# Kernel tuning notes

Hardware: AMD Instinct MI355X
Metric: run time of the kernel (lower is better)

## Reference

```python
import jax, jax.numpy as jnp
import numpy as np

B, L, INPUT_DIM = 2, 2048, 512
D_MODEL, N_HEAD, MLP_HIDDEN = 1024, 16, 4096
CONTEXT_LENGTH = 2048
EPS = 1e-5


def _layer_norm(x, w, b):
    mu = jnp.mean(x, axis=-1, keepdims=True)
    var = jnp.mean(jnp.square(x - mu), axis=-1, keepdims=True)
    return (x - mu) * jax.lax.rsqrt(var + EPS) * w + b


def setup_inputs() -> dict:
    key = jax.random.key(0)
    ks = jax.random.split(key, 12)
    s = 0.02
    return {
        "x": jax.random.normal(ks[0], (B, L, INPUT_DIM), dtype=jnp.float32),
        "wte_w": jax.random.normal(ks[1], (INPUT_DIM, D_MODEL), dtype=jnp.float32) * s,
        "wte_b": jnp.zeros((D_MODEL,), dtype=jnp.float32),
        "wpe": jax.random.normal(ks[2], (CONTEXT_LENGTH, D_MODEL), dtype=jnp.float32) * s,
        "ln1_w": jnp.ones((D_MODEL,), dtype=jnp.float32),
        "ln1_b": jnp.zeros((D_MODEL,), dtype=jnp.float32),
        "kq_w": jax.random.normal(ks[3], (D_MODEL, 2 * D_MODEL), dtype=jnp.float32) * s,
        "kq_b": jnp.zeros((2 * D_MODEL,), dtype=jnp.float32),
        "v_w": jax.random.normal(ks[4], (D_MODEL, D_MODEL), dtype=jnp.float32) * s,
        "v_b": jnp.zeros((D_MODEL,), dtype=jnp.float32),
        "ao_w": jax.random.normal(ks[5], (D_MODEL, D_MODEL), dtype=jnp.float32) * s,
        "ao_b": jnp.zeros((D_MODEL,), dtype=jnp.float32),
        "ln2_w": jnp.ones((D_MODEL,), dtype=jnp.float32),
        "ln2_b": jnp.zeros((D_MODEL,), dtype=jnp.float32),
        "fc_w": jax.random.normal(ks[6], (D_MODEL, MLP_HIDDEN), dtype=jnp.float32) * s,
        "fc_b": jnp.zeros((MLP_HIDDEN,), dtype=jnp.float32),
        "proj_w": jax.random.normal(ks[7], (MLP_HIDDEN, INPUT_DIM), dtype=jnp.float32) * s,
        "proj_b": jnp.zeros((INPUT_DIM,), dtype=jnp.float32),
    }


def reference(x, wte_w, wte_b, wpe, ln1_w, ln1_b, kq_w, kq_b, v_w, v_b,
              ao_w, ao_b, ln2_w, ln2_b, fc_w, fc_b, proj_w, proj_b):
    b, l, _ = x.shape
    hd = D_MODEL // N_HEAD
    # token "embedding" (linear) + learnable positional embedding
    h = x @ wte_w + wte_b + wpe[:l]                      # [B, L, D]
    hn = _layer_norm(h, ln1_w, ln1_b)                    # ln_1
    # attention (kq fused linear -> split gives k first, then q)
    kq = hn @ kq_w + kq_b                                # [B, L, 2D]
    k, q = kq[..., :D_MODEL], kq[..., D_MODEL:]
    v = hn @ v_w + v_b
    q = q.reshape(b, l, N_HEAD, hd).transpose(0, 2, 1, 3)  # [B, H, L, hd]
    k = k.reshape(b, l, N_HEAD, hd).transpose(0, 2, 1, 3)
    v = v.reshape(b, l, N_HEAD, hd).transpose(0, 2, 1, 3)
    scale = 1.0 / jnp.sqrt(jnp.asarray(hd, dtype=q.dtype))
    scores = jnp.einsum('bhqd,bhkd->bhqk', q, k) * scale  # [B, H, L, L]
    causal = jnp.tril(jnp.ones((l, l), dtype=bool))
    scores = jnp.where(causal, scores, jnp.asarray(-jnp.inf, dtype=scores.dtype))
    attn = jax.nn.softmax(scores, axis=-1)
    o = jnp.einsum('bhqk,bhkd->bhqd', attn, v)            # [B, H, L, hd]
    o = o.transpose(0, 2, 1, 3).reshape(b, l, D_MODEL)
    o = o @ ao_w + ao_b
    attn_out = hn + o                                     # residual recorded by Block
    xo = _layer_norm(attn_out, ln2_w, ln2_b)              # ln_2
    # MLP head to input_dim (exact GELU, matching torch nn.GELU default)
    out = jax.nn.gelu(xo @ fc_w + fc_b, approximate=False) @ proj_w + proj_b
    return (out, attn_out)
```

## Files before the change

### kernel.cpp

```cpp
#include <hip/hip_runtime.h>
#include <hip/hip_bf16.h>
#include <cmath>

#define D_MODEL   1024
#define N_HEAD    16
#define HEAD_DIM  64
#define SEQ_LEN   2048
#define NBATCH    2
#define M_TOTAL   (NBATCH * SEQ_LEN)
#define IN_DIM    512
#define MLP_HID   4096

typedef __attribute__((ext_vector_type(8))) short short8;
typedef __attribute__((ext_vector_type(4))) short short4v;
typedef __attribute__((ext_vector_type(4))) float floatx4;

typedef const __attribute__((address_space(1))) void* gas_ptr;
typedef __attribute__((address_space(3))) void* las_ptr;

__device__ __forceinline__ void async_copy16(const void* g, void* l) {
  __builtin_amdgcn_global_load_lds((gas_ptr)g, (las_ptr)l, 16, 0, 0);
}


__global__ __launch_bounds__(256) void k_convert_bf16(const float* __restrict__ in,
                                                      __hip_bfloat16* __restrict__ out,
                                                      int n4) {
  int i = blockIdx.x * 256 + threadIdx.x;
  if (i >= n4) return;
  float4 v = ((const float4*)in)[i];
  int base = i * 4;
  out[base + 0] = __float2bfloat16(v.x);
  out[base + 1] = __float2bfloat16(v.y);
  out[base + 2] = __float2bfloat16(v.z);
  out[base + 3] = __float2bfloat16(v.w);
}

__global__ __launch_bounds__(256) void k_reduce_proj(const __hip_bfloat16* __restrict__ part,
                                                     const float* __restrict__ bias,
                                                     float* __restrict__ out) {
  int i = blockIdx.x * 256 + threadIdx.x;
  const size_t SP = (size_t)M_TOTAL * IN_DIM / 4;
  float4 s = ((const float4*)bias)[i & (IN_DIM / 4 - 1)];
#pragma unroll
  for (int j = 0; j < 8; j++) {
    short4v v = ((const short4v*)part)[i + j * SP];
    s.x += __bfloat162float(((const __hip_bfloat16*)&v)[0]);
    s.y += __bfloat162float(((const __hip_bfloat16*)&v)[1]);
    s.z += __bfloat162float(((const __hip_bfloat16*)&v)[2]);
    s.w += __bfloat162float(((const __hip_bfloat16*)&v)[3]);
  }
  ((float4*)out)[i] = s;
}

__global__ __launch_bounds__(256) void k_transpose_bf16(const float* __restrict__ in,
                                                        __hip_bfloat16* __restrict__ out,
                                                        int K, int N) {
  __shared__ float tile[32][33];
  int n0 = blockIdx.x * 32, k0 = blockIdx.y * 32;
  int tx = threadIdx.x & 31, ty = threadIdx.x >> 5;
#pragma unroll
  for (int i = 0; i < 32; i += 8)
    tile[ty + i][tx] = in[(size_t)(k0 + ty + i) * N + n0 + tx];
  __syncthreads();
#pragma unroll
  for (int i = 0; i < 32; i += 8)
    out[(size_t)(n0 + ty + i) * K + k0 + tx] = __float2bfloat16(tile[tx][ty + i]);
}

__global__ __launch_bounds__(256) void k_transpose_v(const __hip_bfloat16* __restrict__ in,
                                                     __hip_bfloat16* __restrict__ out) {
  __shared__ __hip_bfloat16 t[64][72];
  int bh = blockIdx.y;
  int l0 = blockIdx.x * 64;
  in  += (size_t)bh * SEQ_LEN * HEAD_DIM;
  out += (size_t)bh * HEAD_DIM * SEQ_LEN;
  int tx = threadIdx.x & 7, ty = threadIdx.x >> 3;
#pragma unroll
  for (int i = 0; i < 64; i += 32) {
    short8 v = *(const short8*)(in + (size_t)(l0 + ty + i) * HEAD_DIM + tx * 8);
#pragma unroll
    for (int j = 0; j < 8; j++) t[ty + i][tx * 8 + j] = ((__hip_bfloat16*)&v)[j];
  }
  __syncthreads();
#pragma unroll
  for (int i = 0; i < 64; i += 32) {
    int d = ty + i;
    short8 o;
#pragma unroll
    for (int j = 0; j < 8; j++) ((__hip_bfloat16*)&o)[j] = t[tx * 8 + j][d];
    *(short8*)(out + (size_t)d * SEQ_LEN + l0 + tx * 8) = o;
  }
}


__global__ __launch_bounds__(256) void k_ln1_combine(const float* __restrict__ part,
                                                     const float* __restrict__ wb,
                                                     const float* __restrict__ wpe,
                                                     const float* __restrict__ lw,
                                                     const float* __restrict__ lb,
                                                     __hip_bfloat16* __restrict__ out_bf) {
  int row = blockIdx.x;
  int l = row & (SEQ_LEN - 1);
  float4 a = ((const float4*)(part + (size_t)row * D_MODEL))[threadIdx.x];
  float4 c = ((const float4*)(part + (size_t)(M_TOTAL + row) * D_MODEL))[threadIdx.x];
  float4 wb4 = ((const float4*)wb)[threadIdx.x];
  float4 pe4 = ((const float4*)(wpe + (size_t)l * D_MODEL))[threadIdx.x];
  float4 v;
  v.x = a.x + c.x + wb4.x + pe4.x;
  v.y = a.y + c.y + wb4.y + pe4.y;
  v.z = a.z + c.z + wb4.z + pe4.z;
  v.w = a.w + c.w + wb4.w + pe4.w;
  float s  = v.x + v.y + v.z + v.w;
  float sq = v.x * v.x + v.y * v.y + v.z * v.z + v.w * v.w;
#pragma unroll
  for (int o = 1; o < 64; o <<= 1) { s += __shfl_xor(s, o); sq += __shfl_xor(sq, o); }
  __shared__ float ss[4], ssq[4];
  int lane = threadIdx.x & 63, wv = threadIdx.x >> 6;
  if (lane == 0) { ss[wv] = s; ssq[wv] = sq; }
  __syncthreads();
  s  = ss[0] + ss[1] + ss[2] + ss[3];
  sq = ssq[0] + ssq[1] + ssq[2] + ssq[3];
  float mu  = s * (1.f / D_MODEL);
  float var = sq * (1.f / D_MODEL) - mu * mu;
  float rs  = rsqrtf(var + 1e-5f);
  float4 lw4 = ((const float4*)lw)[threadIdx.x];
  float4 lb4 = ((const float4*)lb)[threadIdx.x];
  size_t base = (size_t)row * D_MODEL + threadIdx.x * 4;
  out_bf[base + 0] = __float2bfloat16((v.x - mu) * rs * lw4.x + lb4.x);
  out_bf[base + 1] = __float2bfloat16((v.y - mu) * rs * lw4.y + lb4.y);
  out_bf[base + 2] = __float2bfloat16((v.z - mu) * rs * lw4.z + lb4.z);
  out_bf[base + 3] = __float2bfloat16((v.w - mu) * rs * lw4.w + lb4.w);
}

__global__ __launch_bounds__(256) void k_ln2_combine(const float* __restrict__ part,
                                                     const float* __restrict__ bias,
                                                     const __hip_bfloat16* __restrict__ hn,
                                                     const float* __restrict__ lw,
                                                     const float* __restrict__ lb,
                                                     float* __restrict__ attn_out,
                                                     __hip_bfloat16* __restrict__ out_bf) {
  int row = blockIdx.x;
  float4 a = ((const float4*)(part + (size_t)row * D_MODEL))[threadIdx.x];
  float4 c = ((const float4*)(part + (size_t)(M_TOTAL + row) * D_MODEL))[threadIdx.x];
  float4 b4 = ((const float4*)bias)[threadIdx.x];
  short4v h4 = ((const short4v*)(hn + (size_t)row * D_MODEL))[threadIdx.x];
  float4 v;
  v.x = a.x + c.x + b4.x + __bfloat162float(((const __hip_bfloat16*)&h4)[0]);
  v.y = a.y + c.y + b4.y + __bfloat162float(((const __hip_bfloat16*)&h4)[1]);
  v.z = a.z + c.z + b4.z + __bfloat162float(((const __hip_bfloat16*)&h4)[2]);
  v.w = a.w + c.w + b4.w + __bfloat162float(((const __hip_bfloat16*)&h4)[3]);
  ((float4*)(attn_out + (size_t)row * D_MODEL))[threadIdx.x] = v;
  float s  = v.x + v.y + v.z + v.w;
  float sq = v.x * v.x + v.y * v.y + v.z * v.z + v.w * v.w;
#pragma unroll
  for (int o = 1; o < 64; o <<= 1) { s += __shfl_xor(s, o); sq += __shfl_xor(sq, o); }
  __shared__ float ss[4], ssq[4];
  int lane = threadIdx.x & 63, wv = threadIdx.x >> 6;
  if (lane == 0) { ss[wv] = s; ssq[wv] = sq; }
  __syncthreads();
  s  = ss[0] + ss[1] + ss[2] + ss[3];
  sq = ssq[0] + ssq[1] + ssq[2] + ssq[3];
  float mu  = s * (1.f / D_MODEL);
  float var = sq * (1.f / D_MODEL) - mu * mu;
  float rs  = rsqrtf(var + 1e-5f);
  float4 lw4 = ((const float4*)lw)[threadIdx.x];
  float4 lb4 = ((const float4*)lb)[threadIdx.x];
  size_t base = (size_t)row * D_MODEL + threadIdx.x * 4;
  out_bf[base + 0] = __float2bfloat16((v.x - mu) * rs * lw4.x + lb4.x);
  out_bf[base + 1] = __float2bfloat16((v.y - mu) * rs * lw4.y + lb4.y);
  out_bf[base + 2] = __float2bfloat16((v.z - mu) * rs * lw4.z + lb4.z);
  out_bf[base + 3] = __float2bfloat16((v.w - mu) * rs * lw4.w + lb4.w);
}


struct KQVEpi {
  const float* kq_b; const float* v_b;
  __hip_bfloat16* kb; __hip_bfloat16* qb; __hip_bfloat16* vb;
  __device__ void operator()(int row, int col, float v) const {
    int b = row >> 11, l = row & (SEQ_LEN - 1);
    int which = col >> 10, c = col & (D_MODEL - 1);
    float t = v + ((which == 2) ? v_b[c] : kq_b[col]);
    if (which == 1) t *= 0.125f;
    int head = c >> 6, d = c & 63;
    __hip_bfloat16* dst = (which == 0) ? kb : (which == 1) ? qb : vb;
    dst[(((size_t)(b * N_HEAD + head) * SEQ_LEN) + l) * HEAD_DIM + d] = __float2bfloat16(t);
  }
};

struct FCEpi {
  const float* bias; __hip_bfloat16* act;
  __device__ void operator()(int row, int col, float v) const {
    float t = v + bias[col];
    float g = 0.5f * t * (1.f + erff(t * 0.70710678118654752f));
    act[(size_t)row * MLP_HID + col] = __float2bfloat16(g);
  }
};

struct PartEpi {
  float* part;
  __device__ void operator()(int row, int col, float v) const {
    part[(size_t)blockIdx.z * ((size_t)M_TOTAL * D_MODEL) + (size_t)row * D_MODEL + col] = v;
  }
};

struct PartBf16Epi {
  __hip_bfloat16* part;
  __device__ void operator()(int row, int col, float v) const {
    part[(size_t)blockIdx.z * ((size_t)M_TOTAL * IN_DIM) + (size_t)row * IN_DIM + col] =
        __float2bfloat16(v);
  }
};


template <class Epi>
__global__ __launch_bounds__(256) void k_gemm(const __hip_bfloat16* __restrict__ A,
                                              const __hip_bfloat16* __restrict__ Bt,
                                              int M, int N, int K, int Kchunk, Epi epi) {
  __shared__ __align__(16) short As[128 * 64];
  __shared__ __align__(16) short Bs[128 * 64];
  const int tid  = threadIdx.x;
  const int lane = tid & 63;
  const int w    = tid >> 6;
  const int wm   = (w >> 1) << 6;
  const int wn   = (w & 1) << 6;
  const int r    = lane & 15;
  const int quad = lane >> 4;
  const int m0 = blockIdx.y << 7;
  const int n0 = blockIdx.x << 7;
  const int koff = blockIdx.z * Kchunk;

  const __hip_bfloat16* pa[4];
  const __hip_bfloat16* pb[4];
#pragma unroll
  for (int j = 0; j < 4; j++) {
    int s = tid + j * 256;
    int row = s >> 3;
    int c = (s & 7) ^ (row & 7);
    pa[j] = A  + (size_t)(m0 + row) * K + (c << 3) + koff;
    pb[j] = Bt + (size_t)(n0 + row) * K + (c << 3) + koff;
  }

  floatx4 acc[4][4];
#pragma unroll
  for (int i = 0; i < 4; i++)
#pragma unroll
    for (int j = 0; j < 4; j++) acc[i][j] = (floatx4){0.f, 0.f, 0.f, 0.f};

  int aoff[2][4], boff[2][4];
#pragma unroll
  for (int kk = 0; kk < 2; kk++)
#pragma unroll
    for (int i = 0; i < 4; i++) {
      int pc = ((quad + (kk << 2)) ^ (r & 7)) << 3;
      aoff[kk][i] = (wm + i * 16 + r) * 64 + pc;
      boff[kk][i] = (wn + i * 16 + r) * 64 + pc;
    }

  for (int k0 = 0; k0 < Kchunk; k0 += 64) {
    __syncthreads();
#pragma unroll
    for (int j = 0; j < 4; j++) {
      async_copy16(pa[j] + k0, &As[(tid + j * 256) * 8]);
      async_copy16(pb[j] + k0, &Bs[(tid + j * 256) * 8]);
    }
    __syncthreads();
#pragma unroll
    for (int kk = 0; kk < 2; kk++) {
      short8 fa[4], fb[4];
#pragma unroll
      for (int i = 0; i < 4; i++) {
        fa[i] = *(const short8*)&As[aoff[kk][i]];
        fb[i] = *(const short8*)&Bs[boff[kk][i]];
      }
#pragma unroll
      for (int i = 0; i < 4; i++)
#pragma unroll
        for (int j = 0; j < 4; j++)
          acc[i][j] = __builtin_amdgcn_mfma_f32_16x16x32_bf16(fa[i], fb[j], acc[i][j], 0, 0, 0);
    }
  }

#pragma unroll
  for (int i = 0; i < 4; i++)
#pragma unroll
    for (int j = 0; j < 4; j++) {
      int row = m0 + wm + i * 16 + quad * 4;
      int col = n0 + wn + j * 16 + r;
#pragma unroll
      for (int t = 0; t < 4; t++) epi(row + t, col, acc[i][j][t]);
    }
}

template <class Epi>
static void launch_gemm(const __hip_bfloat16* A, const __hip_bfloat16* Bt,
                        int M, int N, int K, Epi epi, hipStream_t s) {
  dim3 grid(N / 128, M / 128, 1);
  k_gemm<Epi><<<grid, 256, 0, s>>>(A, Bt, M, N, K, K, epi);
}


#define PSTR 68

__global__ __launch_bounds__(256) void k_flash_attn(const __hip_bfloat16* __restrict__ kb,
                                                    const __hip_bfloat16* __restrict__ qb,
                                                    const __hip_bfloat16* __restrict__ vtb,
                                                    __hip_bfloat16* __restrict__ ob) {
  __shared__ __align__(16) short Ks[64 * 64];
  __shared__ __align__(16) short Vs[64 * 64];
  __shared__ __align__(16) __hip_bfloat16 Pb[4][2][16 * PSTR];
  const int tid  = threadIdx.x;
  const int lane = tid & 63;
  const int w    = tid >> 6;
  const int r    = lane & 15;
  const int quad = lane >> 4;
  const int bh    = blockIdx.x & 31;
  const int strip = (SEQ_LEN / 128 - 1) - (blockIdx.x >> 5);
  const int qb0   = strip << 7;
  const int qbw   = qb0 + (w << 5);
  const int qend  = qbw + 32;
  const int b = bh >> 4, h = bh & (N_HEAD - 1);

  const __hip_bfloat16* qp = qb  + ((size_t)bh * SEQ_LEN + qbw) * HEAD_DIM;
  const __hip_bfloat16* kp = kb  + (size_t)bh * SEQ_LEN * HEAD_DIM;
  const __hip_bfloat16* vp = vtb + (size_t)bh * HEAD_DIM * SEQ_LEN;
  __hip_bfloat16* pw0 = &Pb[w][0][0];
  __hip_bfloat16* pw1 = &Pb[w][1][0];

  short8 qf[2][2];
  qf[0][0] = *(const short8*)(qp + r * HEAD_DIM + quad * 8);
  qf[0][1] = *(const short8*)(qp + r * HEAD_DIM + quad * 8 + 32);
  qf[1][0] = *(const short8*)(qp + (16 + r) * HEAD_DIM + quad * 8);
  qf[1][1] = *(const short8*)(qp + (16 + r) * HEAD_DIM + quad * 8 + 32);

  floatx4 of[2][4];
#pragma unroll
  for (int f = 0; f < 2; f++)
#pragma unroll
    for (int i = 0; i < 4; i++) of[f][i] = (floatx4){0.f, 0.f, 0.f, 0.f};
  float ls0 = 0.f, ls1 = 0.f;

  const int c0 = tid, c1 = tid + 256;
  const int row0 = c0 >> 3, g0 = (c0 & 7) ^ (row0 & 7);
  const int row1 = c1 >> 3, g1 = (c1 & 7) ^ (row1 & 7);
  const int sw = r & 7;

  const int ktiles = (qb0 + 128) >> 6;
  for (int t = 0; t < ktiles; ++t) {
    const int ts = t << 6;
    __syncthreads();
    async_copy16(kp + (size_t)(ts + row0) * HEAD_DIM + g0 * 8, &Ks[c0 * 8]);
    async_copy16(kp + (size_t)(ts + row1) * HEAD_DIM + g1 * 8, &Ks[c1 * 8]);
    async_copy16(vp + (size_t)row0 * SEQ_LEN + ts + g0 * 8, &Vs[c0 * 8]);
    async_copy16(vp + (size_t)row1 * SEQ_LEN + ts + g1 * 8, &Vs[c1 * 8]);
    __syncthreads();
    if (ts >= qend) continue;

#pragma unroll
    for (int kt = 0; kt < 4; kt++) {
      const int tss = ts + (kt << 4);
      short4v pk0, pk1;
      if (tss < qend) {
        const int krow = (kt << 4) + r;
        short8 a0 = *(const short8*)&Ks[(krow * 8 + (quad ^ sw)) * 8];
        short8 a1 = *(const short8*)&Ks[(krow * 8 + ((quad ^ sw) ^ 4)) * 8];
        floatx4 s0 = (floatx4){0.f,0.f,0.f,0.f}, s1 = (floatx4){0.f,0.f,0.f,0.f};
        s0 = __builtin_amdgcn_mfma_f32_16x16x32_bf16(a0, qf[0][0], s0, 0, 0, 0);
        s0 = __builtin_amdgcn_mfma_f32_16x16x32_bf16(a1, qf[0][1], s0, 0, 0, 0);
        s1 = __builtin_amdgcn_mfma_f32_16x16x32_bf16(a0, qf[1][0], s1, 0, 0, 0);
        s1 = __builtin_amdgcn_mfma_f32_16x16x32_bf16(a1, qf[1][1], s1, 0, 0, 0);
        if (tss + 15 > qbw) {
          int off0 = qbw + r - tss;
          int off1 = off0 + 16;
#pragma unroll
          for (int tt = 0; tt < 4; tt++) {
            int kl = (quad << 2) + tt;
            if (kl > off0) s0[tt] = -INFINITY;
            if (kl > off1) s1[tt] = -INFINITY;
          }
        }
#pragma unroll
        for (int tt = 0; tt < 4; tt++) {
          float e0 = __expf(s0[tt]); ls0 += e0;
          float e1 = __expf(s1[tt]); ls1 += e1;
          ((__hip_bfloat16*)&pk0)[tt] = __float2bfloat16(e0);
          ((__hip_bfloat16*)&pk1)[tt] = __float2bfloat16(e1);
        }
      } else {
        pk0 = (short4v){0, 0, 0, 0};
        pk1 = (short4v){0, 0, 0, 0};
      }
      *(short4v*)(pw0 + r * PSTR + (kt << 4) + (quad << 2)) = pk0;
      *(short4v*)(pw1 + r * PSTR + (kt << 4) + (quad << 2)) = pk1;
    }
#pragma unroll
    for (int c = 0; c < 2; c++) {
      short8 pb0 = *(const short8*)(pw0 + r * PSTR + (c << 5) + (quad << 3));
      short8 pb1 = *(const short8*)(pw1 + r * PSTR + (c << 5) + (quad << 3));
#pragma unroll
      for (int fd = 0; fd < 4; fd++) {
        const int vrow = (fd << 4) + r;
        short8 va = *(const short8*)&Vs[(vrow * 8 + (((c << 2) + quad) ^ sw)) * 8];
        of[0][fd] = __builtin_amdgcn_mfma_f32_16x16x32_bf16(va, pb0, of[0][fd], 0, 0, 0);
        of[1][fd] = __builtin_amdgcn_mfma_f32_16x16x32_bf16(va, pb1, of[1][fd], 0, 0, 0);
      }
    }
  }

  ls0 += __shfl_xor(ls0, 16); ls0 += __shfl_xor(ls0, 32);
  ls1 += __shfl_xor(ls1, 16); ls1 += __shfl_xor(ls1, 32);
  float inv0 = 1.f / ls0, inv1 = 1.f / ls1;

#pragma unroll
  for (int f = 0; f < 2; f++) {
    float inv = f ? inv1 : inv0;
    size_t orow = ((size_t)b * SEQ_LEN + qbw + f * 16 + r) * D_MODEL + (size_t)h * HEAD_DIM;
#pragma unroll
    for (int fd = 0; fd < 4; fd++) {
      short4v o4;
#pragma unroll
      for (int tt = 0; tt < 4; tt++)
        ((__hip_bfloat16*)&o4)[tt] = __float2bfloat16(of[f][fd][tt] * inv);
      *(short4v*)(ob + orow + fd * 16 + quad * 4) = o4;
    }
  }
}


extern "C" void kernel_launch(void* const* d_in, const int* in_sizes, int n_in,
                              void* d_out, int out_size, void* d_ws, size_t ws_size,
                              hipStream_t stream) {
  (void)in_sizes; (void)n_in; (void)out_size; (void)ws_size;
  const float* x      = (const float*)d_in[0];
  const float* wte_w  = (const float*)d_in[1];
  const float* wte_b  = (const float*)d_in[2];
  const float* wpe    = (const float*)d_in[3];
  const float* ln1_w  = (const float*)d_in[4];
  const float* ln1_b  = (const float*)d_in[5];
  const float* kq_w   = (const float*)d_in[6];
  const float* kq_b   = (const float*)d_in[7];
  const float* v_w    = (const float*)d_in[8];
  const float* v_b    = (const float*)d_in[9];
  const float* ao_w   = (const float*)d_in[10];
  const float* ao_b   = (const float*)d_in[11];
  const float* ln2_w  = (const float*)d_in[12];
  const float* ln2_b  = (const float*)d_in[13];
  const float* fc_w   = (const float*)d_in[14];
  const float* fc_b   = (const float*)d_in[15];
  const float* proj_w = (const float*)d_in[16];
  const float* proj_b = (const float*)d_in[17];

  float* out0     = (float*)d_out;
  float* attn_out = out0 + (size_t)M_TOTAL * IN_DIM;

  char* ws = (char*)d_ws;
  const size_t MB8 = (size_t)M_TOTAL * D_MODEL * 2;
  __hip_bfloat16* wT    = (__hip_bfloat16*)ws;
  __hip_bfloat16* x_bf  = (__hip_bfloat16*)(ws + 8 * 1048576);
  char* R1              = ws + 12 * 1048576;
  float* embed_part     = (float*)R1;
  float* ao_part        = (float*)R1;
  __hip_bfloat16* act   = (__hip_bfloat16*)R1;
  __hip_bfloat16* k_bf  = (__hip_bfloat16*)(ws + 44 * 1048576);
  __hip_bfloat16* q_bf  = (__hip_bfloat16*)(ws + 52 * 1048576);
  __hip_bfloat16* v_bf  = (__hip_bfloat16*)(ws + 60 * 1048576);
  __hip_bfloat16* vt_bf = (__hip_bfloat16*)(ws + 68 * 1048576);
  __hip_bfloat16* o_bf  = (__hip_bfloat16*)(ws + 76 * 1048576);
  __hip_bfloat16* hn_bf = (__hip_bfloat16*)(ws + 84 * 1048576);
  __hip_bfloat16* xo_bf = k_bf;
  __hip_bfloat16* proj_part = k_bf;
  (void)MB8;

  k_convert_bf16<<<(M_TOTAL * IN_DIM / 4 + 255) / 256, 256, 0, stream>>>(x, x_bf, M_TOTAL * IN_DIM / 4);

  k_transpose_bf16<<<dim3(D_MODEL / 32, IN_DIM / 32), 256, 0, stream>>>(wte_w, wT, IN_DIM, D_MODEL);
  {
    dim3 grid(D_MODEL / 128, M_TOTAL / 128, 2);
    k_gemm<PartEpi><<<grid, 256, 0, stream>>>(x_bf, wT, M_TOTAL, D_MODEL, IN_DIM, IN_DIM / 2,
                                              PartEpi{embed_part});
  }

  k_ln1_combine<<<M_TOTAL, 256, 0, stream>>>(embed_part, wte_b, wpe, ln1_w, ln1_b, hn_bf);

  k_transpose_bf16<<<dim3(2 * D_MODEL / 32, D_MODEL / 32), 256, 0, stream>>>(kq_w, wT, D_MODEL, 2 * D_MODEL);
  k_transpose_bf16<<<dim3(D_MODEL / 32, D_MODEL / 32), 256, 0, stream>>>(v_w, wT + (size_t)2 * D_MODEL * D_MODEL, D_MODEL, D_MODEL);
  launch_gemm(hn_bf, wT, M_TOTAL, 3 * D_MODEL, D_MODEL,
              KQVEpi{kq_b, v_b, k_bf, q_bf, v_bf}, stream);
  k_transpose_v<<<dim3(SEQ_LEN / 64, NBATCH * N_HEAD), 256, 0, stream>>>(v_bf, vt_bf);

  k_flash_attn<<<(SEQ_LEN / 128) * 32, 256, 0, stream>>>(k_bf, q_bf, vt_bf, o_bf);

  k_transpose_bf16<<<dim3(D_MODEL / 32, D_MODEL / 32), 256, 0, stream>>>(ao_w, wT, D_MODEL, D_MODEL);
  {
    dim3 grid(D_MODEL / 128, M_TOTAL / 128, 2);
    k_gemm<PartEpi><<<grid, 256, 0, stream>>>(o_bf, wT, M_TOTAL, D_MODEL, D_MODEL, D_MODEL / 2,
                                              PartEpi{ao_part});
  }

  k_ln2_combine<<<M_TOTAL, 256, 0, stream>>>(ao_part, ao_b, hn_bf, ln2_w, ln2_b, attn_out, xo_bf);

  k_transpose_bf16<<<dim3(MLP_HID / 32, D_MODEL / 32), 256, 0, stream>>>(fc_w, wT, D_MODEL, MLP_HID);
  launch_gemm(xo_bf, wT, M_TOTAL, MLP_HID, D_MODEL, FCEpi{fc_b, act}, stream);

  k_transpose_bf16<<<dim3(IN_DIM / 32, MLP_HID / 32), 256, 0, stream>>>(proj_w, wT, MLP_HID, IN_DIM);
  {
    dim3 grid(IN_DIM / 128, M_TOTAL / 128, 8);
    k_gemm<PartBf16Epi><<<grid, 256, 0, stream>>>(act, wT, M_TOTAL, IN_DIM, MLP_HID, MLP_HID / 8,
                                                  PartBf16Epi{proj_part});
  }
  k_reduce_proj<<<M_TOTAL * IN_DIM / 4 / 256, 256, 0, stream>>>(proj_part, proj_b, out0);
}
```

Before: 425.3 us.

## Replace GEMM with 256x256-tile, 8-wave, double-buffered pipelined kernel

Swaps the 128x128 single-buffered bf16 MFMA GEMM for a 256x256-tile kernel with 512 threads and double-buffered LDS. Async global-to-LDS prefetch of later K tiles is interleaved with MFMA sub-blocks, using explicit barriers, waitcnt and s_setprio. The aim is to hide load latency and raise data reuse per tile. In exchange the grids shrink to 128–256 blocks, which may leave CUs idle on the smaller GEMMs. The 128KB of LDS per block also likely limits occupancy to one block per CU.

```diff
diff --git a/kernel.cpp b/kernel.cpp
--- a/kernel.cpp
+++ b/kernel.cpp
@@ -213,90 +213,155 @@
 };
 
 
+#define STAGE_A(BUF, H, KT)                                                       \
+  do {                                                                            \
+    async_copy16(ga + (size_t)((H) * 128) * K + (KT) * 64,                        \
+                 &As[BUF][(tid + (H) * 1024) * 8]);                               \
+    async_copy16(ga + (size_t)((H) * 128 + 64) * K + (KT) * 64,                   \
+                 &As[BUF][(tid + (H) * 1024 + 512) * 8]);                         \
+  } while (0)
+
+#define STAGE_B(BUF, H, KT)                                                       \
+  do {                                                                            \
+    async_copy16(gb + (size_t)((H) * 128) * K + (KT) * 64,                        \
+                 &Bs[BUF][(tid + (H) * 1024) * 8]);                               \
+    async_copy16(gb + (size_t)((H) * 128 + 64) * K + (KT) * 64,                   \
+                 &Bs[BUF][(tid + (H) * 1024 + 512) * 8]);                         \
+  } while (0)
+
+#define MFMA_BLK(IO, JO, BFX)                                                     \
+  _Pragma("unroll") for (int i = 0; i < 4; i++) {                                 \
+    _Pragma("unroll") for (int j = 0; j < 2; j++) {                               \
+      acc[(IO) + i][(JO) + j] = __builtin_amdgcn_mfma_f32_16x16x32_bf16(          \
+          af[i][0], BFX[j][0], acc[(IO) + i][(JO) + j], 0, 0, 0);                 \
+      acc[(IO) + i][(JO) + j] = __builtin_amdgcn_mfma_f32_16x16x32_bf16(          \
+          af[i][1], BFX[j][1], acc[(IO) + i][(JO) + j], 0, 0, 0);                 \
+    }                                                                             \
+  }
+
+#define GTILE(T, BUF)                                                             \
+  {                                                                               \
+                                    \
+    _Pragma("unroll") for (int i = 0; i < 4; i++) {                               \
+      af[i][0] = *(const short8*)&As[BUF][arb[i] + pc0];                          \
+      af[i][1] = *(const short8*)&As[BUF][arb[i] + pc1];                          \
+    }                                                                             \
+    _Pragma("unroll") for (int j = 0; j < 2; j++) {                               \
+      bf0[j][0] = *(const short8*)&Bs[BUF][brb[j] + pc0];                         \
+      bf0[j][1] = *(const short8*)&Bs[BUF][brb[j] + pc1];                         \
+    }                                                                             \
+    if ((T) + 1 < nt) { STAGE_A((BUF) ^ 1, 1, (T) + 1); }                         \
+    __builtin_amdgcn_s_barrier();                                                 \
+    asm volatile("s_waitcnt lgkmcnt(0)" ::: "memory");                            \
+    __builtin_amdgcn_s_setprio(1);                                                \
+    MFMA_BLK(0, 0, bf0)                                                           \
+    __builtin_amdgcn_s_setprio(0);                                                \
+    __builtin_amdgcn_s_barrier();                                                 \
+                                           \
+    _Pragma("unroll") for (int j = 0; j < 2; j++) {                               \
+      bf1[j][0] = *(const short8*)&Bs[BUF][brb[j] + 8192 + pc0];                  \
+      bf1[j][1] = *(const short8*)&Bs[BUF][brb[j] + 8192 + pc1];                  \
+    }                                                                             \
+    if ((T) + 2 < nt) { STAGE_A(BUF, 0, (T) + 2); }                               \
+    __builtin_amdgcn_s_barrier();                                                 \
+    asm volatile("s_waitcnt lgkmcnt(0)" ::: "memory");                            \
+    __builtin_amdgcn_s_setprio(1);                                                \
+    MFMA_BLK(0, 2, bf1)                                                           \
+    __builtin_amdgcn_s_setprio(0);                                                \
+    __builtin_amdgcn_s_barrier();                                                 \
+                                           \
+    _Pragma("unroll") for (int i = 0; i < 4; i++) {                               \
+      af[i][0] = *(const short8*)&As[BUF][arb[i] + 8192 + pc0];                   \
+      af[i][1] = *(const short8*)&As[BUF][arb[i] + 8192 + pc1];                   \
+    }                                                                             \
+    if ((T) + 2 < nt) { STAGE_B(BUF, 0, (T) + 2); }                               \
+    __builtin_amdgcn_s_barrier();                                                 \
+    asm volatile("s_waitcnt lgkmcnt(0)" ::: "memory");                            \
+    __builtin_amdgcn_s_setprio(1);                                                \
+    MFMA_BLK(4, 0, bf0)                                                           \
+    __builtin_amdgcn_s_setprio(0);                                                \
+    __builtin_amdgcn_s_barrier();                                                 \
+                    \
+    if ((T) + 2 < nt) { STAGE_B(BUF, 1, (T) + 2); }                               \
+    __builtin_amdgcn_s_setprio(1);                                                \
+    MFMA_BLK(4, 2, bf1)                                                           \
+    __builtin_amdgcn_s_setprio(0);                                                \
+    if ((T) + 2 < nt) {                                                           \
+      asm volatile("s_waitcnt vmcnt(6)" ::: "memory");                            \
+    } else {                                                                      \
+      asm volatile("s_waitcnt vmcnt(0)" ::: "memory");                            \
+    }                                                                             \
+    __builtin_amdgcn_s_barrier();                                                 \
+  }
+
 template <class Epi>
-__global__ __launch_bounds__(256) void k_gemm(const __hip_bfloat16* __restrict__ A,
-                                              const __hip_bfloat16* __restrict__ Bt,
-                                              int M, int N, int K, int Kchunk, Epi epi) {
-  __shared__ __align__(16) short As[128 * 64];
-  __shared__ __align__(16) short Bs[128 * 64];
+__global__ __launch_bounds__(512, 2) void k_gemm256(const __hip_bfloat16* __restrict__ A,
+                                                    const __hip_bfloat16* __restrict__ Bt,
+                                                    int M, int N, int K, int Kchunk, Epi epi) {
+  (void)M; (void)N;
+  __shared__ __align__(16) short As[2][16384];
+  __shared__ __align__(16) short Bs[2][16384];
   const int tid  = threadIdx.x;
   const int lane = tid & 63;
   const int w    = tid >> 6;
-  const int wm   = (w >> 1) << 6;
-  const int wn   = (w & 1) << 6;
+  const int wr   = w >> 2;
+  const int wc   = w & 3;
   const int r    = lane & 15;
   const int quad = lane >> 4;
-  const int m0 = blockIdx.y << 7;
-  const int n0 = blockIdx.x << 7;
+  const int m0 = blockIdx.y << 8;
+  const int n0 = blockIdx.x << 8;
   const int koff = blockIdx.z * Kchunk;
-
-  const __hip_bfloat16* pa[4];
-  const __hip_bfloat16* pb[4];
-#pragma unroll
-  for (int j = 0; j < 4; j++) {
-    int s = tid + j * 256;
-    int row = s >> 3;
-    int c = (s & 7) ^ (row & 7);
-    pa[j] = A  + (size_t)(m0 + row) * K + (c << 3) + koff;
-    pb[j] = Bt + (size_t)(n0 + row) * K + (c << 3) + koff;
-  }
-
-  floatx4 acc[4][4];
-#pragma unroll
-  for (int i = 0; i < 4; i++)
+  const int nt = Kchunk >> 6;
+
+  const int sr = tid >> 3;
+  const int sc = (tid & 7) ^ (sr & 7);
+  const __hip_bfloat16* ga = A  + (size_t)(m0 + sr) * K + sc * 8 + koff;
+  const __hip_bfloat16* gb = Bt + (size_t)(n0 + sr) * K + sc * 8 + koff;
+
+  const int pc0 = ((quad    ) ^ (r & 7)) << 3;
+  const int pc1 = ((quad + 4) ^ (r & 7)) << 3;
+  int arb[4], brb[2];
+#pragma unroll
+  for (int i = 0; i < 4; i++) arb[i] = ((2 * i + wr) * 16 + r) * 64;
+#pragma unroll
+  for (int j = 0; j < 2; j++) brb[j] = ((4 * j + wc) * 16 + r) * 64;
+
+  floatx4 acc[8][4];
+#pragma unroll
+  for (int i = 0; i < 8; i++)
 #pragma unroll
     for (int j = 0; j < 4; j++) acc[i][j] = (floatx4){0.f, 0.f, 0.f, 0.f};
-
-  int aoff[2][4], boff[2][4];
-#pragma unroll
-  for (int kk = 0; kk < 2; kk++)
-#pragma unroll
-    for (int i = 0; i < 4; i++) {
-      int pc = ((quad + (kk << 2)) ^ (r & 7)) << 3;
-      aoff[kk][i] = (wm + i * 16 + r) * 64 + pc;
-      boff[kk][i] = (wn + i * 16 + r) * 64 + pc;
+  short8 af[4][2], bf0[2][2], bf1[2][2];
+
+  STAGE_A(0, 0, 0);
+  STAGE_B(0, 0, 0);
+  STAGE_B(0, 1, 0);
+  STAGE_A(0, 1, 0);
+  if (nt > 1) {
+    STAGE_A(1, 0, 1);
+    STAGE_B(1, 0, 1);
+    STAGE_B(1, 1, 1);
+    asm volatile("s_waitcnt vmcnt(6)" ::: "memory");
+  } else {
+    asm volatile("s_waitcnt vmcnt(0)" ::: "memory");
+  }
+  __builtin_amdgcn_s_barrier();
+
+  for (int t = 0; t < nt; t += 2) {
+    GTILE(t, 0)
+    GTILE(t + 1, 1)
+  }
+
+#pragma unroll
+  for (int i = 0; i < 8; i++) {
+    int row = m0 + (2 * i + wr) * 16 + quad * 4;
+#pragma unroll
+    for (int j = 0; j < 4; j++) {
+      int col = n0 + (4 * j + wc) * 16 + r;
+#pragma unroll
+      for (int tt = 0; tt < 4; tt++) epi(row + tt, col, acc[i][j][tt]);
     }
-
-  for (int k0 = 0; k0 < Kchunk; k0 += 64) {
-    __syncthreads();
-#pragma unroll
-    for (int j = 0; j < 4; j++) {
-      async_copy16(pa[j] + k0, &As[(tid + j * 256) * 8]);
-      async_copy16(pb[j] + k0, &Bs[(tid + j * 256) * 8]);
-    }
-    __syncthreads();
-#pragma unroll
-    for (int kk = 0; kk < 2; kk++) {
-      short8 fa[4], fb[4];
-#pragma unroll
-      for (int i = 0; i < 4; i++) {
-        fa[i] = *(const short8*)&As[aoff[kk][i]];
-        fb[i] = *(const short8*)&Bs[boff[kk][i]];
-      }
-#pragma unroll
-      for (int i = 0; i < 4; i++)
-#pragma unroll
-        for (int j = 0; j < 4; j++)
-          acc[i][j] = __builtin_amdgcn_mfma_f32_16x16x32_bf16(fa[i], fb[j], acc[i][j], 0, 0, 0);
-    }
-  }
-
-#pragma unroll
-  for (int i = 0; i < 4; i++)
-#pragma unroll
-    for (int j = 0; j < 4; j++) {
-      int row = m0 + wm + i * 16 + quad * 4;
-      int col = n0 + wn + j * 16 + r;
-#pragma unroll
-      for (int t = 0; t < 4; t++) epi(row + t, col, acc[i][j][t]);
-    }
-}
-
-template <class Epi>
-static void launch_gemm(const __hip_bfloat16* A, const __hip_bfloat16* Bt,
-                        int M, int N, int K, Epi epi, hipStream_t s) {
-  dim3 grid(N / 128, M / 128, 1);
-  k_gemm<Epi><<<grid, 256, 0, s>>>(A, Bt, M, N, K, K, epi);
+  }
 }
 
 
@@ -475,38 +540,45 @@
 
   k_transpose_bf16<<<dim3(D_MODEL / 32, IN_DIM / 32), 256, 0, stream>>>(wte_w, wT, IN_DIM, D_MODEL);
   {
-    dim3 grid(D_MODEL / 128, M_TOTAL / 128, 2);
-    k_gemm<PartEpi><<<grid, 256, 0, stream>>>(x_bf, wT, M_TOTAL, D_MODEL, IN_DIM, IN_DIM / 2,
-                                              PartEpi{embed_part});
+    dim3 grid(D_MODEL / 256, M_TOTAL / 256, 2);
+    k_gemm256<PartEpi><<<grid, 512, 0, stream>>>(x_bf, wT, M_TOTAL, D_MODEL, IN_DIM, IN_DIM / 2,
+                                                 PartEpi{embed_part});
   }
 
   k_ln1_combine<<<M_TOTAL, 256, 0, stream>>>(embed_part, wte_b, wpe, ln1_w, ln1_b, hn_bf);
 
   k_transpose_bf16<<<dim3(2 * D_MODEL / 32, D_MODEL / 32), 256, 0, stream>>>(kq_w, wT, D_MODEL, 2 * D_MODEL);
   k_transpose_bf16<<<dim3(D_MODEL / 32, D_MODEL / 32), 256, 0, stream>>>(v_w, wT + (size_t)2 * D_MODEL * D_MODEL, D_MODEL, D_MODEL);
-  launch_gemm(hn_bf, wT, M_TOTAL, 3 * D_MODEL, D_MODEL,
-              KQVEpi{kq_b, v_b, k_bf, q_bf, v_bf}, stream);
+  {
+    dim3 grid(3 * D_MODEL / 256, M_TOTAL / 256, 1);
+    k_gemm256<KQVEpi><<<grid, 512, 0, stream>>>(hn_bf, wT, M_TOTAL, 3 * D_MODEL, D_MODEL, D_MODEL,
+                                                KQVEpi{kq_b, v_b, k_bf, q_bf, v_bf});
+  }
   k_transpose_v<<<dim3(SEQ_LEN / 64, NBATCH * N_HEAD), 256, 0, stream>>>(v_bf, vt_bf);
 
   k_flash_attn<<<(SEQ_LEN / 128) * 32, 256, 0, stream>>>(k_bf, q_bf, vt_bf, o_bf);
 
   k_transpose_bf16<<<dim3(D_MODEL / 32, D_MODEL / 32), 256, 0, stream>>>(ao_w, wT, D_MODEL, D_MODEL);
   {
-    dim3 grid(D_MODEL / 128, M_TOTAL / 128, 2);
-    k_gemm<PartEpi><<<grid, 256, 0, stream>>>(o_bf, wT, M_TOTAL, D_MODEL, D_MODEL, D_MODEL / 2,
-                                              PartEpi{ao_part});
+    dim3 grid(D_MODEL / 256, M_TOTAL / 256, 2);
+    k_gemm256<PartEpi><<<grid, 512, 0, stream>>>(o_bf, wT, M_TOTAL, D_MODEL, D_MODEL, D_MODEL / 2,
+                                                 PartEpi{ao_part});
   }
 
   k_ln2_combine<<<M_TOTAL, 256, 0, stream>>>(ao_part, ao_b, hn_bf, ln2_w, ln2_b, attn_out, xo_bf);
 
   k_transpose_bf16<<<dim3(MLP_HID / 32, D_MODEL / 32), 256, 0, stream>>>(fc_w, wT, D_MODEL, MLP_HID);
-  launch_gemm(xo_bf, wT, M_TOTAL, MLP_HID, D_MODEL, FCEpi{fc_b, act}, stream);
+  {
+    dim3 grid(MLP_HID / 256, M_TOTAL / 256, 1);
+    k_gemm256<FCEpi><<<grid, 512, 0, stream>>>(xo_bf, wT, M_TOTAL, MLP_HID, D_MODEL, D_MODEL,
+                                               FCEpi{fc_b, act});
+  }
 
   k_transpose_bf16<<<dim3(IN_DIM / 32, MLP_HID / 32), 256, 0, stream>>>(proj_w, wT, MLP_HID, IN_DIM);
   {
-    dim3 grid(IN_DIM / 128, M_TOTAL / 128, 8);
-    k_gemm<PartBf16Epi><<<grid, 256, 0, stream>>>(act, wT, M_TOTAL, IN_DIM, MLP_HID, MLP_HID / 8,
-                                                  PartBf16Epi{proj_part});
+    dim3 grid(IN_DIM / 256, M_TOTAL / 256, 8);
+    k_gemm256<PartBf16Epi><<<grid, 512, 0, stream>>>(act, wT, M_TOTAL, IN_DIM, MLP_HID, MLP_HID / 8,
+                                                     PartBf16Epi{proj_part});
   }
   k_reduce_proj<<<M_TOTAL * IN_DIM / 4 / 256, 256, 0, stream>>>(proj_part, proj_b, out0);
 }
```

After: 413.8 us. -2.7%, faster.

## Double-buffer flash attention K/V tiles with 8 waves; fp32 4-way proj split-K

Applied to the files above, without the earlier changes.

The flash attention kernel now runs 512 threads, with each wave handling 16 query rows instead of 32. K/V tiles are double-buffered in LDS: the tile two steps ahead is prefetched asynchronously while the current one is computed, using explicit vmcnt waits and raw barriers in place of the per-tile __syncthreads. This is meant to hide global load latency and raise the number of waves available to the scheduler. Separately, the projection GEMM split-K drops from 8 to 4 partitions and stores fp32 partials instead of bf16, which changes reduction traffic and improves accuracy but gives each block a longer K loop and so less parallelism.

```diff
diff --git a/kernel.cpp b/kernel.cpp
--- a/kernel.cpp
+++ b/kernel.cpp
@@ -36,19 +36,16 @@
   out[base + 3] = __float2bfloat16(v.w);
 }
 
-__global__ __launch_bounds__(256) void k_reduce_proj(const __hip_bfloat16* __restrict__ part,
-                                                     const float* __restrict__ bias,
-                                                     float* __restrict__ out) {
+__global__ __launch_bounds__(256) void k_reduce_proj4(const float* __restrict__ part,
+                                                      const float* __restrict__ bias,
+                                                      float* __restrict__ out) {
   int i = blockIdx.x * 256 + threadIdx.x;
   const size_t SP = (size_t)M_TOTAL * IN_DIM / 4;
   float4 s = ((const float4*)bias)[i & (IN_DIM / 4 - 1)];
 #pragma unroll
-  for (int j = 0; j < 8; j++) {
-    short4v v = ((const short4v*)part)[i + j * SP];
-    s.x += __bfloat162float(((const __hip_bfloat16*)&v)[0]);
-    s.y += __bfloat162float(((const __hip_bfloat16*)&v)[1]);
-    s.z += __bfloat162float(((const __hip_bfloat16*)&v)[2]);
-    s.w += __bfloat162float(((const __hip_bfloat16*)&v)[3]);
+  for (int j = 0; j < 4; j++) {
+    float4 v = ((const float4*)part)[i + j * SP];
+    s.x += v.x; s.y += v.y; s.z += v.z; s.w += v.w;
   }
   ((float4*)out)[i] = s;
 }
@@ -204,11 +201,10 @@
   }
 };
 
-struct PartBf16Epi {
-  __hip_bfloat16* part;
+struct PartProjEpi {
+  float* part;
   __device__ void operator()(int row, int col, float v) const {
-    part[(size_t)blockIdx.z * ((size_t)M_TOTAL * IN_DIM) + (size_t)row * IN_DIM + col] =
-        __float2bfloat16(v);
+    part[(size_t)blockIdx.z * ((size_t)M_TOTAL * IN_DIM) + (size_t)row * IN_DIM + col] = v;
   }
 };
 
@@ -302,127 +298,125 @@
 
 #define PSTR 68
 
-__global__ __launch_bounds__(256) void k_flash_attn(const __hip_bfloat16* __restrict__ kb,
-                                                    const __hip_bfloat16* __restrict__ qb,
-                                                    const __hip_bfloat16* __restrict__ vtb,
-                                                    __hip_bfloat16* __restrict__ ob) {
-  __shared__ __align__(16) short Ks[64 * 64];
-  __shared__ __align__(16) short Vs[64 * 64];
-  __shared__ __align__(16) __hip_bfloat16 Pb[4][2][16 * PSTR];
+#define STAGE_KV(T, P)                                                         \
+  do {                                                                         \
+    async_copy16(kp + (size_t)((((T) << 6)) + srow) * HEAD_DIM + sg * 8,       \
+                 &Ks[P][tid * 8]);                                             \
+    async_copy16(vp + (size_t)srow * SEQ_LEN + ((T) << 6) + sg * 8,            \
+                 &Vs[P][tid * 8]);                                             \
+  } while (0)
+
+#define ATILE(T, P)                                                            \
+  {                                                                            \
+    const int ts = (T) << 6;                                                   \
+    if (ts < qend) {                                                           \
+      _Pragma("unroll") for (int kt = 0; kt < 4; kt++) {                       \
+        const int tss = ts + (kt << 4);                                        \
+        short4v pk0;                                                           \
+        if (tss < qend) {                                                      \
+          const int krow = (kt << 4) + r;                                      \
+          short8 a0 = *(const short8*)&Ks[P][(krow * 8 + (quad ^ sw)) * 8];    \
+          short8 a1 = *(const short8*)&Ks[P][(krow * 8 + ((quad ^ sw) ^ 4)) * 8]; \
+          floatx4 s0 = (floatx4){0.f, 0.f, 0.f, 0.f};                          \
+          s0 = __builtin_amdgcn_mfma_f32_16x16x32_bf16(a0, qf0, s0, 0, 0, 0);  \
+          s0 = __builtin_amdgcn_mfma_f32_16x16x32_bf16(a1, qf1, s0, 0, 0, 0);  \
+          if (tss + 15 > qbw) {                                                \
+            int off0 = qbw + r - tss;                                          \
+            _Pragma("unroll") for (int tt = 0; tt < 4; tt++) {                 \
+              int kl = (quad << 2) + tt;                                       \
+              if (kl > off0) s0[tt] = -INFINITY;                               \
+            }                                                                  \
+          }                                                                    \
+          _Pragma("unroll") for (int tt = 0; tt < 4; tt++) {                   \
+            float e0 = __expf(s0[tt]); ls0 += e0;                              \
+            ((__hip_bfloat16*)&pk0)[tt] = __float2bfloat16(e0);                \
+          }                                                                    \
+        } else {                                                               \
+          pk0 = (short4v){0, 0, 0, 0};                                         \
+        }                                                                      \
+        *(short4v*)(pw + r * PSTR + (kt << 4) + (quad << 2)) = pk0;            \
+      }                                                                        \
+      __builtin_amdgcn_s_setprio(1);                                           \
+      _Pragma("unroll") for (int c = 0; c < 2; c++) {                          \
+        short8 pb0 = *(const short8*)(pw + r * PSTR + (c << 5) + (quad << 3)); \
+        _Pragma("unroll") for (int fd = 0; fd < 4; fd++) {                     \
+          const int vrow = (fd << 4) + r;                                      \
+          short8 va = *(const short8*)&Vs[P][(vrow * 8 + (((c << 2) + quad) ^ sw)) * 8]; \
+          of[fd] = __builtin_amdgcn_mfma_f32_16x16x32_bf16(va, pb0, of[fd], 0, 0, 0); \
+        }                                                                      \
+      }                                                                        \
+      __builtin_amdgcn_s_setprio(0);                                           \
+    }                                                                          \
+    __builtin_amdgcn_s_barrier();                                              \
+    if ((T) + 2 < ktiles) {                                                    \
+      STAGE_KV((T) + 2, P);                                                    \
+      asm volatile("s_waitcnt vmcnt(2)" ::: "memory");                         \
+    } else {                                                                   \
+      asm volatile("s_waitcnt vmcnt(0)" ::: "memory");                         \
+    }                                                                          \
+    __builtin_amdgcn_s_barrier();                                              \
+    __builtin_amdgcn_sched_barrier(0);                                         \
+  }
+
+__global__ __launch_bounds__(512, 4) void k_flash_attn(const __hip_bfloat16* __restrict__ kb,
+                                                       const __hip_bfloat16* __restrict__ qb,
+                                                       const __hip_bfloat16* __restrict__ vtb,
+                                                       __hip_bfloat16* __restrict__ ob) {
+  __shared__ __align__(16) short Ks[2][64 * 64];
+  __shared__ __align__(16) short Vs[2][64 * 64];
+  __shared__ __align__(16) __hip_bfloat16 Pb[8][16 * PSTR];
   const int tid  = threadIdx.x;
   const int lane = tid & 63;
   const int w    = tid >> 6;
   const int r    = lane & 15;
   const int quad = lane >> 4;
+  const int sw   = r & 7;
   const int bh    = blockIdx.x & 31;
   const int strip = (SEQ_LEN / 128 - 1) - (blockIdx.x >> 5);
   const int qb0   = strip << 7;
-  const int qbw   = qb0 + (w << 5);
-  const int qend  = qbw + 32;
+  const int qbw   = qb0 + (w << 4);
+  const int qend  = qbw + 16;
   const int b = bh >> 4, h = bh & (N_HEAD - 1);
 
   const __hip_bfloat16* qp = qb  + ((size_t)bh * SEQ_LEN + qbw) * HEAD_DIM;
   const __hip_bfloat16* kp = kb  + (size_t)bh * SEQ_LEN * HEAD_DIM;
   const __hip_bfloat16* vp = vtb + (size_t)bh * HEAD_DIM * SEQ_LEN;
-  __hip_bfloat16* pw0 = &Pb[w][0][0];
-  __hip_bfloat16* pw1 = &Pb[w][1][0];
-
-  short8 qf[2][2];
-  qf[0][0] = *(const short8*)(qp + r * HEAD_DIM + quad * 8);
-  qf[0][1] = *(const short8*)(qp + r * HEAD_DIM + quad * 8 + 32);
-  qf[1][0] = *(const short8*)(qp + (16 + r) * HEAD_DIM + quad * 8);
-  qf[1][1] = *(const short8*)(qp + (16 + r) * HEAD_DIM + quad * 8 + 32);
-
-  floatx4 of[2][4];
-#pragma unroll
-  for (int f = 0; f < 2; f++)
-#pragma unroll
-    for (int i = 0; i < 4; i++) of[f][i] = (floatx4){0.f, 0.f, 0.f, 0.f};
-  float ls0 = 0.f, ls1 = 0.f;
-
-  const int c0 = tid, c1 = tid + 256;
-  const int row0 = c0 >> 3, g0 = (c0 & 7) ^ (row0 & 7);
-  const int row1 = c1 >> 3, g1 = (c1 & 7) ^ (row1 & 7);
-  const int sw = r & 7;
+  __hip_bfloat16* pw = &Pb[w][0];
+
+  short8 qf0 = *(const short8*)(qp + r * HEAD_DIM + quad * 8);
+  short8 qf1 = *(const short8*)(qp + r * HEAD_DIM + quad * 8 + 32);
+
+  floatx4 of[4];
+#pragma unroll
+  for (int i = 0; i < 4; i++) of[i] = (floatx4){0.f, 0.f, 0.f, 0.f};
+  float ls0 = 0.f;
+
+  const int srow = tid >> 3;
+  const int sg = (tid & 7) ^ (srow & 7);
 
   const int ktiles = (qb0 + 128) >> 6;
-  for (int t = 0; t < ktiles; ++t) {
-    const int ts = t << 6;
-    __syncthreads();
-    async_copy16(kp + (size_t)(ts + row0) * HEAD_DIM + g0 * 8, &Ks[c0 * 8]);
-    async_copy16(kp + (size_t)(ts + row1) * HEAD_DIM + g1 * 8, &Ks[c1 * 8]);
-    async_copy16(vp + (size_t)row0 * SEQ_LEN + ts + g0 * 8, &Vs[c0 * 8]);
-    async_copy16(vp + (size_t)row1 * SEQ_LEN + ts + g1 * 8, &Vs[c1 * 8]);
-    __syncthreads();
-    if (ts >= qend) continue;
-
-#pragma unroll
-    for (int kt = 0; kt < 4; kt++) {
-      const int tss = ts + (kt << 4);
-      short4v pk0, pk1;
-      if (tss < qend) {
-        const int krow = (kt << 4) + r;
-        short8 a0 = *(const short8*)&Ks[(krow * 8 + (quad ^ sw)) * 8];
-        short8 a1 = *(const short8*)&Ks[(krow * 8 + ((quad ^ sw) ^ 4)) * 8];
-        floatx4 s0 = (floatx4){0.f,0.f,0.f,0.f}, s1 = (floatx4){0.f,0.f,0.f,0.f};
-        s0 = __builtin_amdgcn_mfma_f32_16x16x32_bf16(a0, qf[0][0], s0, 0, 0, 0);
-        s0 = __builtin_amdgcn_mfma_f32_16x16x32_bf16(a1, qf[0][1], s0, 0, 0, 0);
-        s1 = __builtin_amdgcn_mfma_f32_16x16x32_bf16(a0, qf[1][0], s1, 0, 0, 0);
-        s1 = __builtin_amdgcn_mfma_f32_16x16x32_bf16(a1, qf[1][1], s1, 0, 0, 0);
-        if (tss + 15 > qbw) {
-          int off0 = qbw + r - tss;
-          int off1 = off0 + 16;
-#pragma unroll
-          for (int tt = 0; tt < 4; tt++) {
-            int kl = (quad << 2) + tt;
-            if (kl > off0) s0[tt] = -INFINITY;
-            if (kl > off1) s1[tt] = -INFINITY;
-          }
-        }
-#pragma unroll
-        for (int tt = 0; tt < 4; tt++) {
-          float e0 = __expf(s0[tt]); ls0 += e0;
-          float e1 = __expf(s1[tt]); ls1 += e1;
-          ((__hip_bfloat16*)&pk0)[tt] = __float2bfloat16(e0);
-          ((__hip_bfloat16*)&pk1)[tt] = __float2bfloat16(e1);
-        }
-      } else {
-        pk0 = (short4v){0, 0, 0, 0};
-        pk1 = (short4v){0, 0, 0, 0};
-      }
-      *(short4v*)(pw0 + r * PSTR + (kt << 4) + (quad << 2)) = pk0;
-      *(short4v*)(pw1 + r * PSTR + (kt << 4) + (quad << 2)) = pk1;
-    }
-#pragma unroll
-    for (int c = 0; c < 2; c++) {
-      short8 pb0 = *(const short8*)(pw0 + r * PSTR + (c << 5) + (quad << 3));
-      short8 pb1 = *(const short8*)(pw1 + r * PSTR + (c << 5) + (quad << 3));
-#pragma unroll
-      for (int fd = 0; fd < 4; fd++) {
-        const int vrow = (fd << 4) + r;
-        short8 va = *(const short8*)&Vs[(vrow * 8 + (((c << 2) + quad) ^ sw)) * 8];
-        of[0][fd] = __builtin_amdgcn_mfma_f32_16x16x32_bf16(va, pb0, of[0][fd], 0, 0, 0);
-        of[1][fd] = __builtin_amdgcn_mfma_f32_16x16x32_bf16(va, pb1, of[1][fd], 0, 0, 0);
-      }
-    }
+  STAGE_KV(0, 0);
+  STAGE_KV(1, 1);
+  asm volatile("s_waitcnt vmcnt(2)" ::: "memory");
+  __builtin_amdgcn_s_barrier();
+  __builtin_amdgcn_sched_barrier(0);
+
+  for (int t = 0; t < ktiles; t += 2) {
+    ATILE(t, 0)
+    ATILE(t + 1, 1)
   }
 
   ls0 += __shfl_xor(ls0, 16); ls0 += __shfl_xor(ls0, 32);
-  ls1 += __shfl_xor(ls1, 16); ls1 += __shfl_xor(ls1, 32);
-  float inv0 = 1.f / ls0, inv1 = 1.f / ls1;
-
-#pragma unroll
-  for (int f = 0; f < 2; f++) {
-    float inv = f ? inv1 : inv0;
-    size_t orow = ((size_t)b * SEQ_LEN + qbw + f * 16 + r) * D_MODEL + (size_t)h * HEAD_DIM;
-#pragma unroll
-    for (int fd = 0; fd < 4; fd++) {
-      short4v o4;
-#pragma unroll
-      for (int tt = 0; tt < 4; tt++)
-        ((__hip_bfloat16*)&o4)[tt] = __float2bfloat16(of[f][fd][tt] * inv);
-      *(short4v*)(ob + orow + fd * 16 + quad * 4) = o4;
-    }
+  float inv0 = 1.f / ls0;
+
+  size_t orow = ((size_t)b * SEQ_LEN + qbw + r) * D_MODEL + (size_t)h * HEAD_DIM;
+#pragma unroll
+  for (int fd = 0; fd < 4; fd++) {
+    short4v o4;
+#pragma unroll
+    for (int tt = 0; tt < 4; tt++)
+      ((__hip_bfloat16*)&o4)[tt] = __float2bfloat16(of[fd][tt] * inv0);
+    *(short4v*)(ob + orow + fd * 16 + quad * 4) = o4;
   }
 }
 
@@ -454,7 +448,6 @@
   float* attn_out = out0 + (size_t)M_TOTAL * IN_DIM;
 
   char* ws = (char*)d_ws;
-  const size_t MB8 = (size_t)M_TOTAL * D_MODEL * 2;
   __hip_bfloat16* wT    = (__hip_bfloat16*)ws;
   __hip_bfloat16* x_bf  = (__hip_bfloat16*)(ws + 8 * 1048576);
   char* R1              = ws + 12 * 1048576;
@@ -468,8 +461,7 @@
   __hip_bfloat16* o_bf  = (__hip_bfloat16*)(ws + 76 * 1048576);
   __hip_bfloat16* hn_bf = (__hip_bfloat16*)(ws + 84 * 1048576);
   __hip_bfloat16* xo_bf = k_bf;
-  __hip_bfloat16* proj_part = k_bf;
-  (void)MB8;
+  float* proj_part      = (float*)(ws + 44 * 1048576);
 
   k_convert_bf16<<<(M_TOTAL * IN_DIM / 4 + 255) / 256, 256, 0, stream>>>(x, x_bf, M_TOTAL * IN_DIM / 4);
 
@@ -488,7 +480,7 @@
               KQVEpi{kq_b, v_b, k_bf, q_bf, v_bf}, stream);
   k_transpose_v<<<dim3(SEQ_LEN / 64, NBATCH * N_HEAD), 256, 0, stream>>>(v_bf, vt_bf);
 
-  k_flash_attn<<<(SEQ_LEN / 128) * 32, 256, 0, stream>>>(k_bf, q_bf, vt_bf, o_bf);
+  k_flash_attn<<<(SEQ_LEN / 128) * 32, 512, 0, stream>>>(k_bf, q_bf, vt_bf, o_bf);
 
   k_transpose_bf16<<<dim3(D_MODEL / 32, D_MODEL / 32), 256, 0, stream>>>(ao_w, wT, D_MODEL, D_MODEL);
   {
@@ -504,9 +496,9 @@
 
   k_transpose_bf16<<<dim3(IN_DIM / 32, MLP_HID / 32), 256, 0, stream>>>(proj_w, wT, MLP_HID, IN_DIM);
   {
-    dim3 grid(IN_DIM / 128, M_TOTAL / 128, 8);
-    k_gemm<PartBf16Epi><<<grid, 256, 0, stream>>>(act, wT, M_TOTAL, IN_DIM, MLP_HID, MLP_HID / 8,
-                                                  PartBf16Epi{proj_part});
-  }
-  k_reduce_proj<<<M_TOTAL * IN_DIM / 4 / 256, 256, 0, stream>>>(proj_part, proj_b, out0);
-}
+    dim3 grid(IN_DIM / 128, M_TOTAL / 128, 4);
+    k_gemm<PartProjEpi><<<grid, 256, 0, stream>>>(act, wT, M_TOTAL, IN_DIM, MLP_HID, MLP_HID / 4,
+                                                  PartProjEpi{proj_part});
+  }
+  k_reduce_proj4<<<M_TOTAL * IN_DIM / 4 / 256, 256, 0, stream>>>(proj_part, proj_b, out0);
+}
```

Result: faster. 409.3 us (-3.8%).
